# Optimization experiments

Hardware: AMD Instinct MI355X
Metric: run time of the kernel (lower is better)

Reference implementation:

```python
import jax, jax.numpy as jnp
import numpy as np

B, S, D, H = 2, 2048, 1024, 16
DK = D // H  # 64


def setup_inputs() -> dict:
    key = jax.random.key(0)
    ks = jax.random.split(key, 8)
    q = jax.random.normal(ks[0], (B, S, D), dtype=jnp.float32)
    k = jax.random.normal(ks[1], (B, S, D), dtype=jnp.float32)
    v = jax.random.normal(ks[2], (B, S, D), dtype=jnp.float32)
    mask = jax.random.randint(ks[3], (B, 1, S, S), 0, 2, dtype=jnp.int32)
    scale = 1.0 / np.sqrt(D)
    Wq = jax.random.normal(ks[4], (D, D), dtype=jnp.float32) * scale
    Wk = jax.random.normal(ks[5], (D, D), dtype=jnp.float32) * scale
    Wv = jax.random.normal(ks[6], (D, D), dtype=jnp.float32) * scale
    Wo = jax.random.normal(ks[7], (D, D), dtype=jnp.float32) * scale
    return {"q": q, "k": k, "v": v, "mask": mask,
            "Wq": Wq, "Wk": Wk, "Wv": Wv, "Wo": Wo}


def reference(q, k, v, mask, Wq, Wk, Wv, Wo):
    # Linear projections (torch nn.Linear: x @ W.T, no bias)
    qh = (q @ Wq.T).reshape(B, S, H, DK).transpose(0, 2, 1, 3)  # [B,H,S,DK]
    kh = (k @ Wk.T).reshape(B, S, H, DK).transpose(0, 2, 1, 3)
    vh = (v @ Wv.T).reshape(B, S, H, DK).transpose(0, 2, 1, 3)
    # Scaled dot-product attention with mask fill of -1e9 where mask == 0
    scores = jnp.einsum('bhqd,bhkd->bhqk', qh, kh) / jnp.sqrt(jnp.float32(DK))
    scores = jnp.where(mask == 0, jnp.float32(-1e9), scores)
    attn = jax.nn.softmax(scores, axis=-1)
    ctx = jnp.einsum('bhqk,bhkd->bhqd', attn, vh)  # [B,H,S,DK]
    ctx = ctx.transpose(0, 2, 1, 3).reshape(B, S, D)
    return ctx @ Wo.T
```

## Files before the change

### kernel.cpp

```cpp
#include <hip/hip_runtime.h>

using u16    = unsigned short;
using u32    = unsigned int;
using f32x4  = __attribute__((ext_vector_type(4))) float;
using f32x16 = __attribute__((ext_vector_type(16))) float;
using bf16x8 = __attribute__((ext_vector_type(8))) __bf16;
using u16x4  = __attribute__((ext_vector_type(4))) u16;
using u16x8  = __attribute__((ext_vector_type(8))) u16;
using u32x2  = __attribute__((ext_vector_type(2))) u32;
using u32x4  = __attribute__((ext_vector_type(4))) u32;
using i32x4  = __attribute__((ext_vector_type(4))) int;


__device__ __forceinline__ u16 f2bf(float f) {
  union { __bf16 b; u16 u; } c; c.b = (__bf16)f; return c.u;
}

typedef __attribute__((address_space(1))) const void GVoid;
typedef __attribute__((address_space(3))) void LVoid;

__device__ __forceinline__ void gload_lds16(const void* g, void* l) {
  __builtin_amdgcn_global_load_lds((GVoid*)g, (LVoid*)l, 16, 0, 0);
}

__global__ void cvt_w(const float* __restrict__ a, const float* __restrict__ b,
                      const float* __restrict__ c, const float* __restrict__ dd,
                      u16* __restrict__ oa, u16* __restrict__ ob,
                      u16* __restrict__ oc, u16* __restrict__ od) {
  int y = blockIdx.y;
  const float* s = (y == 0) ? a : (y == 1) ? b : (y == 2) ? c : dd;
  u16* d = (y == 0) ? oa : (y == 1) ? ob : (y == 2) ? oc : od;
  int i = blockIdx.x * 256 + threadIdx.x;
  f32x4 v = ((const f32x4*)s)[i];
  u16x4 r;
#pragma unroll
  for (int j = 0; j < 4; ++j) r[j] = f2bf(v[j]);
  ((u16x4*)d)[i] = r;
}

__global__ void pack_mask(const int* __restrict__ m, u32* __restrict__ mp) {
  int tid = blockIdx.x * 256 + threadIdx.x;
  int q = tid & 2047, kt = (tid >> 11) & 31, b = tid >> 16;
  const i32x4* src = (const i32x4*)(m + ((size_t)(b * 2048 + q)) * 2048 + kt * 64);
  u32 w0 = 0, w1 = 0;
#pragma unroll
  for (int j = 0; j < 8; ++j) {
    i32x4 a = src[j], c = src[j + 8];
#pragma unroll
    for (int e = 0; e < 4; ++e) {
      w0 |= (a[e] != 0 ? 1u : 0u) << (j * 4 + e);
      w1 |= (c[e] != 0 ? 1u : 0u) << (j * 4 + e);
    }
  }
  ((u32x2*)mp)[((size_t)(b * 32 + kt)) * 2048 + q] = u32x2{w0, w1};
}

__global__ __launch_bounds__(256, 3) void gemm_qkv(const float* __restrict__ Aq,
                                                   const float* __restrict__ Ak,
                                                   const float* __restrict__ Av,
                                                   const u16* __restrict__ Wb,
                                                   u16* __restrict__ out) {
  __shared__ alignas(16) char lds[49152];
  const int t = threadIdx.x;
  const int lane = t & 63, wid = t >> 6;
  const int g = lane >> 4, r16 = lane & 15;
  const int wm = wid >> 1, wn = wid & 1;
  const int m0 = blockIdx.x * 128, n0 = blockIdx.y * 128;
  const int z = blockIdx.z;

  const float* Axf = (z == 0) ? Aq : (z == 1) ? Ak : Av;
  const char* Ab = (const char*)Axf;
  const char* Bb = (const char*)(Wb + (size_t)z * 1048576);
  u16* op = out + (size_t)z * 4194304;
  const float qsc = (z == 0) ? 0.18033688011f : 1.0f;

  f32x4 acc[4][4] = {};

  for (int kk = 0; kk < 1024; kk += 64) {
#pragma unroll
    for (int i = 0; i < 8; ++i) {
      int ci = i * 256 + t;
      int row = ci >> 4;
      int pc = ci & 15;
      int lc = pc ^ (row & 15);
      gload_lds16(Ab + (size_t)(m0 + row) * 4096 + kk * 4 + lc * 16, lds + ci * 16);
    }
#pragma unroll
    for (int i = 0; i < 4; ++i) {
      int ci = i * 256 + t;
      int row = ci >> 3;
      int cbs = ((ci & 7) << 4) ^ ((row & 7) << 4);
      gload_lds16(Bb + (size_t)(n0 + row) * 2048 + kk * 2 + cbs, lds + 32768 + ci * 16);
    }
    __syncthreads();
#pragma unroll
    for (int kc = 0; kc < 2; ++kc) {
      bf16x8 af[4], bfr[4];
#pragma unroll
      for (int mf = 0; mf < 4; ++mf) {
        int row = wm * 64 + mf * 16 + r16;
        const char* arow = lds + row * 256;
        int x = row & 15;
        int lc0 = 8 * kc + 2 * g;
        f32x4 alo = *(const f32x4*)(arow + ((lc0 ^ x) * 16));
        f32x4 ahi = *(const f32x4*)(arow + (((lc0 + 1) ^ x) * 16));
        u16x8 pk;
#pragma unroll
        for (int j = 0; j < 4; ++j) { pk[j] = f2bf(alo[j]); pk[4 + j] = f2bf(ahi[j]); }
        af[mf] = __builtin_bit_cast(bf16x8, pk);
      }
#pragma unroll
      for (int nf = 0; nf < 4; ++nf) {
        int row = wn * 64 + nf * 16 + r16;
        bfr[nf] = *(const bf16x8*)(lds + 32768 + row * 128 +
                                   ((64 * kc + 16 * g) ^ ((row & 7) << 4)));
      }
#pragma unroll
      for (int mf = 0; mf < 4; ++mf)
#pragma unroll
        for (int nf = 0; nf < 4; ++nf)
          acc[mf][nf] = __builtin_amdgcn_mfma_f32_16x16x32_bf16(af[mf], bfr[nf], acc[mf][nf], 0, 0, 0);
    }
    __syncthreads();
  }

#pragma unroll
  for (int mf = 0; mf < 4; ++mf) {
#pragma unroll
    for (int nf = 0; nf < 4; ++nf) {
      int mb = m0 + wm * 64 + mf * 16 + 4 * g;
      int n = n0 + wn * 64 + nf * 16 + r16;
      if (z == 0) {
        int bb = mb >> 11, h = n >> 6, dk = n & 63;
#pragma unroll
        for (int r = 0; r < 4; ++r) {
          int s2 = (mb + r) & 2047;
          op[((size_t)(bb * 16 + h) * 2048 + s2) * 64 + dk] = f2bf(acc[mf][nf][r] * qsc);
        }
      } else if (z == 1) {
        int h = n >> 6, dk = n & 63;
#pragma unroll
        for (int r = 0; r < 4; ++r) {
          int m = mb + r;
          int bb = m >> 11, s2 = m & 2047;
          size_t off16 = ((((size_t)(bb * 16 + h) * 32 + (s2 >> 6)) * 2 + ((s2 >> 5) & 1)) * 8 +
                          (dk >> 3)) * 32 + (s2 & 31);
          op[off16 * 8 + (dk & 7)] = f2bf(acc[mf][nf][r]);
        }
      } else {
        int bb = mb >> 11, s2 = mb & 2047, h = n >> 6, d = n & 63;
        size_t off16 = ((((size_t)(bb * 16 + h) * 32 + (s2 >> 6)) * 8 + ((s2 & 63) >> 3)) * 2 +
                        (d >> 5)) * 32 + (d & 31);
        u16x4 pv;
#pragma unroll
        for (int r = 0; r < 4; ++r) pv[r] = f2bf(acc[mf][nf][r]);
        *(u16x4*)(op + off16 * 8 + (s2 & 7)) = pv;
      }
    }
  }
}

__global__ __launch_bounds__(256, 2) void gemm_out(const u16* __restrict__ X,
                                                   const u16* __restrict__ W,
                                                   float* __restrict__ out) {
  __shared__ alignas(16) char lds[24576];
  const int t = threadIdx.x;
  const int lane = t & 63, wid = t >> 6;
  const int g = lane >> 4, r16 = lane & 15;
  const int m0 = blockIdx.x * 64, n0 = blockIdx.y * 128;
  const char* Ab = (const char*)X;
  const char* Bb = (const char*)W;

  f32x4 acc[4][2] = {};

  for (int kk = 0; kk < 1024; kk += 64) {
#pragma unroll
    for (int i = 0; i < 2; ++i) {
      int ci = i * 256 + t;
      int row = ci >> 3;
      int cbs = ((ci & 7) << 4) ^ ((row & 7) << 4);
      gload_lds16(Ab + (size_t)(m0 + row) * 2048 + kk * 2 + cbs, lds + ci * 16);
    }
#pragma unroll
    for (int i = 0; i < 4; ++i) {
      int ci = i * 256 + t;
      int row = ci >> 3;
      int cbs = ((ci & 7) << 4) ^ ((row & 7) << 4);
      gload_lds16(Bb + (size_t)(n0 + row) * 2048 + kk * 2 + cbs, lds + 8192 + ci * 16);
    }
    __syncthreads();
#pragma unroll
    for (int kc = 0; kc < 2; ++kc) {
      bf16x8 af[4], bfr[2];
#pragma unroll
      for (int mf = 0; mf < 4; ++mf) {
        int row = mf * 16 + r16;
        af[mf] = *(const bf16x8*)(lds + row * 128 + ((64 * kc + 16 * g) ^ ((row & 7) << 4)));
      }
#pragma unroll
      for (int nf = 0; nf < 2; ++nf) {
        int row = wid * 32 + nf * 16 + r16;
        bfr[nf] = *(const bf16x8*)(lds + 8192 + row * 128 + ((64 * kc + 16 * g) ^ ((row & 7) << 4)));
      }
#pragma unroll
      for (int mf = 0; mf < 4; ++mf)
#pragma unroll
        for (int nf = 0; nf < 2; ++nf)
          acc[mf][nf] = __builtin_amdgcn_mfma_f32_16x16x32_bf16(af[mf], bfr[nf], acc[mf][nf], 0, 0, 0);
    }
    __syncthreads();
  }

#pragma unroll
  for (int mf = 0; mf < 4; ++mf)
#pragma unroll
    for (int nf = 0; nf < 2; ++nf) {
      int mb = m0 + mf * 16 + 4 * g;
      int n = n0 + wid * 32 + nf * 16 + r16;
#pragma unroll
      for (int r = 0; r < 4; ++r) out[(size_t)(mb + r) * 1024 + n] = acc[mf][nf][r];
    }
}

struct KH { bf16x8 k[4]; };

__device__ __forceinline__ void loadKh(KH& f, const char* p) {
#pragma unroll
  for (int c = 0; c < 4; ++c) f.k[c] = *(const bf16x8*)(p + c * 1024);
}

__device__ __forceinline__ void sm_cvt(f32x16& s, u32 wm, float& lr, u32 (&w)[8]) {
  float ps = 0.f;
#pragma unroll
  for (int r = 0; r < 16; ++r) {
    const int bit = (r & 3) + 8 * (r >> 2);
    float p = __builtin_amdgcn_exp2f(s[r]);
    int sm = ((int)(wm << (31 - bit))) >> 31;
    p = __uint_as_float(__float_as_uint(p) & (u32)sm);
    s[r] = p;
    ps += p;
  }
  lr += ps;
#pragma unroll
  for (int ss = 0; ss < 2; ++ss) {
    u32 A0, B0, A1, B1;
    asm("v_cvt_pk_bf16_f32 %0, %1, %2" : "=v"(A0) : "v"(s[8*ss+0]), "v"(s[8*ss+1]));
    asm("v_cvt_pk_bf16_f32 %0, %1, %2" : "=v"(B0) : "v"(s[8*ss+2]), "v"(s[8*ss+3]));
    asm("v_cvt_pk_bf16_f32 %0, %1, %2" : "=v"(A1) : "v"(s[8*ss+4]), "v"(s[8*ss+5]));
    asm("v_cvt_pk_bf16_f32 %0, %1, %2" : "=v"(B1) : "v"(s[8*ss+6]), "v"(s[8*ss+7]));
    asm("v_permlane32_swap_b32 %0, %1" : "+v"(A0), "+v"(A1));
    asm("v_permlane32_swap_b32 %0, %1" : "+v"(B0), "+v"(B1));
    w[4*ss+0] = A0; w[4*ss+1] = B0; w[4*ss+2] = A1; w[4*ss+3] = B1;
  }
}

__device__ __forceinline__ void attn_body(const bf16x8 (&qfa)[4], const bf16x8 (&qfb)[4],
                                          KH& cur, KH& nxt,
                                          const char*& kp, const char*& vp,
                                          const u32x2*& mpa, const u32x2*& mpb,
                                          u32x2& mca, u32x2& mcb,
                                          int kh, int hi,
                                          f32x16& oa0, f32x16& oa1,
                                          f32x16& ob0, f32x16& ob1,
                                          float& lra, float& lrb) {
  bf16x8 v00 = *(const bf16x8*)(vp);
  bf16x8 v01 = *(const bf16x8*)(vp + 512);
  bf16x8 v10 = *(const bf16x8*)(vp + 2048);
  bf16x8 v11 = *(const bf16x8*)(vp + 2560);
  loadKh(nxt, kp);
  u32x2 mna = *mpa;
  u32x2 mnb = *mpb;
  kp += 8192; vp += 8192; mpa += 2048; mpb += 2048;
  __builtin_amdgcn_sched_barrier(0);

  f32x16 sa = {}, sb = {};
#pragma unroll
  for (int c = 0; c < 4; ++c) {
    sa = __builtin_amdgcn_mfma_f32_32x32x16_bf16(cur.k[c], qfa[c], sa, 0, 0, 0);
    sb = __builtin_amdgcn_mfma_f32_32x32x16_bf16(cur.k[c], qfb[c], sb, 0, 0, 0);
  }

  u32 wma = (kh ? mca.y : mca.x) >> (4 * hi);
  u32 wmb = (kh ? mcb.y : mcb.x) >> (4 * hi);
  u32 wa[8], wb[8];
  sm_cvt(sa, wma, lra, wa);
  sm_cvt(sb, wmb, lrb, wb);

  bf16x8 pa0 = __builtin_bit_cast(bf16x8, u32x4{wa[0], wa[1], wa[2], wa[3]});
  bf16x8 pa1 = __builtin_bit_cast(bf16x8, u32x4{wa[4], wa[5], wa[6], wa[7]});
  bf16x8 pb0 = __builtin_bit_cast(bf16x8, u32x4{wb[0], wb[1], wb[2], wb[3]});
  bf16x8 pb1 = __builtin_bit_cast(bf16x8, u32x4{wb[4], wb[5], wb[6], wb[7]});
  oa0 = __builtin_amdgcn_mfma_f32_32x32x16_bf16(pa0, v00, oa0, 0, 0, 0);
  ob0 = __builtin_amdgcn_mfma_f32_32x32x16_bf16(pb0, v00, ob0, 0, 0, 0);
  oa1 = __builtin_amdgcn_mfma_f32_32x32x16_bf16(pa0, v01, oa1, 0, 0, 0);
  ob1 = __builtin_amdgcn_mfma_f32_32x32x16_bf16(pb0, v01, ob1, 0, 0, 0);
  oa0 = __builtin_amdgcn_mfma_f32_32x32x16_bf16(pa1, v10, oa0, 0, 0, 0);
  ob0 = __builtin_amdgcn_mfma_f32_32x32x16_bf16(pb1, v10, ob0, 0, 0, 0);
  oa1 = __builtin_amdgcn_mfma_f32_32x32x16_bf16(pa1, v11, oa1, 0, 0, 0);
  ob1 = __builtin_amdgcn_mfma_f32_32x32x16_bf16(pb1, v11, ob1, 0, 0, 0);
  mca = mna;
  mcb = mnb;
}

__global__ __launch_bounds__(256, 2) void attn_kern(const u16* __restrict__ Qh,
                                                    const u16* __restrict__ Kh,
                                                    const u16* __restrict__ Vt,
                                                    const u32* __restrict__ mp,
                                                    u16* __restrict__ ctx) {
  __shared__ float cmb[2][2][32][64];
  __shared__ float cmbl[2][2][64];
  const int t = threadIdx.x;
  const int wid = t >> 6, lane = t & 63;
  const int qw = wid & 1, kh = wid >> 1;
  const int hi = lane >> 5, l31 = lane & 31;

  const int wg = (blockIdx.x & 7) * 64 + (blockIdx.x >> 3);
  const int qt = wg & 15, bh = wg >> 4;
  const int b = bh >> 4, h = bh & 15;

  const char* qbytes = (const char*)Qh;
  const int qbase_a = qt * 128 + qw * 64;
  const int qbase_b = qbase_a + 32;
  const int qga = qbase_a + l31;
  const int qgb = qbase_b + l31;

  bf16x8 qfa[4], qfb[4];
#pragma unroll
  for (int c = 0; c < 4; ++c) {
    qfa[c] = *(const bf16x8*)(qbytes + ((size_t)bh * 2048 + qga) * 128 + 32 * c + 16 * hi);
    qfb[c] = *(const bf16x8*)(qbytes + ((size_t)bh * 2048 + qgb) * 128 + 32 * c + 16 * hi);
  }

  const char* kp = (const char*)Kh + (size_t)bh * 262144 + kh * 4096 + hi * 512 + l31 * 16;
  const char* vp = (const char*)Vt + (size_t)bh * 262144 + (size_t)(4 * kh + hi) * 1024 + l31 * 16;
  const u32x2* mpa = (const u32x2*)mp + (size_t)b * 65536 + qga;
  const u32x2* mpb = (const u32x2*)mp + (size_t)b * 65536 + qgb;

  f32x16 oa0 = {}, oa1 = {}, ob0 = {}, ob1 = {};
  float lra = 0.f, lrb = 0.f;

  KH A, B2;
  loadKh(A, kp);
  kp += 8192;
  u32x2 mca = *mpa;
  u32x2 mcb = *mpb;
  mpa += 2048; mpb += 2048;

#pragma unroll 1
  for (int it = 0; it < 16; ++it) {
    attn_body(qfa, qfb, A, B2, kp, vp, mpa, mpb, mca, mcb, kh, hi, oa0, oa1, ob0, ob1, lra, lrb);
    attn_body(qfa, qfb, B2, A, kp, vp, mpa, mpb, mca, mcb, kh, hi, oa0, oa1, ob0, ob1, lra, lrb);
  }

  lra += __shfl_xor(lra, 32, 64);
  lrb += __shfl_xor(lrb, 32, 64);

  if (kh) {
#pragma unroll
    for (int r = 0; r < 16; ++r) {
      cmb[qw][0][r][lane]      = oa0[r];
      cmb[qw][0][16 + r][lane] = oa1[r];
      cmb[qw][1][r][lane]      = ob0[r];
      cmb[qw][1][16 + r][lane] = ob1[r];
    }
    cmbl[qw][0][lane] = lra;
    cmbl[qw][1][lane] = lrb;
  }
  __syncthreads();
  if (!kh) {
#pragma unroll
    for (int r = 0; r < 16; ++r) {
      oa0[r] += cmb[qw][0][r][lane];
      oa1[r] += cmb[qw][0][16 + r][lane];
      ob0[r] += cmb[qw][1][r][lane];
      ob1[r] += cmb[qw][1][16 + r][lane];
    }
    lra += cmbl[qw][0][lane];
    lrb += cmbl[qw][1][lane];

    float rla = 1.f / lra, rlb = 1.f / lrb;
#pragma unroll
    for (int r = 0; r < 16; ++r) {
      int crow = (r & 3) + 8 * (r >> 2) + 4 * hi;
      float rva = __shfl(rla, crow, 64);
      float rvb = __shfl(rlb, crow, 64);
      size_t rowa = ((size_t)b * 2048 + qbase_a + crow) * 1024 + h * 64 + l31;
      size_t rowb = ((size_t)b * 2048 + qbase_b + crow) * 1024 + h * 64 + l31;
      ctx[rowa]      = f2bf(oa0[r] * rva);
      ctx[rowa + 32] = f2bf(oa1[r] * rva);
      ctx[rowb]      = f2bf(ob0[r] * rvb);
      ctx[rowb + 32] = f2bf(ob1[r] * rvb);
    }
  }
}

extern "C" void kernel_launch(void* const* d_in, const int* in_sizes, int n_in,
                              void* d_out, int out_size, void* d_ws, size_t ws_size,
                              hipStream_t stream) {
  const float* q  = (const float*)d_in[0];
  const float* k  = (const float*)d_in[1];
  const float* v  = (const float*)d_in[2];
  const int* mask = (const int*)d_in[3];
  const float* Wq = (const float*)d_in[4];
  const float* Wk = (const float*)d_in[5];
  const float* Wv = (const float*)d_in[6];
  const float* Wo = (const float*)d_in[7];

  u16* ws = (u16*)d_ws;
  const size_t NX = (size_t)4096 * 1024;
  const size_t NW = (size_t)1024 * 1024;
  u16* Wqb = ws + 3 * NX;
  u16* Qh  = Wqb + 4 * NW;
  u16* ctx = Qh + 3 * NX;
  u32* mpk = (u32*)ws;

  cvt_w<<<dim3(1024, 4), 256, 0, stream>>>(Wq, Wk, Wv, Wo,
                                           Wqb, Wqb + NW, Wqb + 2 * NW, Wqb + 3 * NW);
  pack_mask<<<dim3(512), 256, 0, stream>>>(mask, mpk);
  gemm_qkv<<<dim3(32, 8, 3), 256, 0, stream>>>(q, k, v, Wqb, Qh);
  attn_kern<<<dim3(512), 256, 0, stream>>>(Qh, Qh + NX, Qh + 2 * NX, mpk, ctx);
  gemm_out<<<dim3(64, 8), 256, 0, stream>>>(ctx, Wqb + 3 * NW, (float*)d_out);
}
```

Measured before the change: 119.3 us.

## Pre-convert Q/K/V activations to bf16 before the QKV projection GEMM

Activations q, k and v are converted to bf16 in a merged conversion kernel together with the weights, and the QKV GEMM now loads bf16 tiles for both operands. This halves the A-tile LDS footprint and global traffic inside the GEMM and removes the per-fragment fp32-to-bf16 packing in its inner loop. In exchange the conversion pass writes and re-reads an extra 24MB of bf16 activations. The workspace region shared with the packed mask is reused, so pack_mask is moved after the GEMM. Launch bounds drop from 3 to 2 blocks per SM.

```diff
diff --git a/kernel.cpp b/kernel.cpp
--- a/kernel.cpp
+++ b/kernel.cpp
@@ -23,19 +23,31 @@
   __builtin_amdgcn_global_load_lds((GVoid*)g, (LVoid*)l, 16, 0, 0);
 }
 
-__global__ void cvt_w(const float* __restrict__ a, const float* __restrict__ b,
-                      const float* __restrict__ c, const float* __restrict__ dd,
-                      u16* __restrict__ oa, u16* __restrict__ ob,
-                      u16* __restrict__ oc, u16* __restrict__ od) {
-  int y = blockIdx.y;
-  const float* s = (y == 0) ? a : (y == 1) ? b : (y == 2) ? c : dd;
-  u16* d = (y == 0) ? oa : (y == 1) ? ob : (y == 2) ? oc : od;
-  int i = blockIdx.x * 256 + threadIdx.x;
-  f32x4 v = ((const f32x4*)s)[i];
+__global__ void cvt_all(const float* __restrict__ q, const float* __restrict__ k,
+                        const float* __restrict__ v, const float* __restrict__ wq,
+                        const float* __restrict__ wk, const float* __restrict__ wv,
+                        const float* __restrict__ wo,
+                        u16* __restrict__ oq, u16* __restrict__ ok, u16* __restrict__ ov,
+                        u16* __restrict__ owq, u16* __restrict__ owk,
+                        u16* __restrict__ owv, u16* __restrict__ owo) {
+  size_t u = (size_t)blockIdx.x * 256 + threadIdx.x;
+  const float* s; u16* d; size_t off;
+  int sel = (int)(u >> 20);
+  if (sel < 3) {
+    s = sel == 0 ? q : sel == 1 ? k : v;
+    d = sel == 0 ? oq : sel == 1 ? ok : ov;
+    off = u & 1048575;
+  } else {
+    int wsel = (int)(u >> 18) & 3;
+    s = wsel == 0 ? wq : wsel == 1 ? wk : wsel == 2 ? wv : wo;
+    d = wsel == 0 ? owq : wsel == 1 ? owk : wsel == 2 ? owv : owo;
+    off = u & 262143;
+  }
+  f32x4 x = ((const f32x4*)s)[off];
   u16x4 r;
 #pragma unroll
-  for (int j = 0; j < 4; ++j) r[j] = f2bf(v[j]);
-  ((u16x4*)d)[i] = r;
+  for (int j = 0; j < 4; ++j) r[j] = f2bf(x[j]);
+  ((u16x4*)d)[off] = r;
 }
 
 __global__ void pack_mask(const int* __restrict__ m, u32* __restrict__ mp) {
@@ -55,12 +67,10 @@
   ((u32x2*)mp)[((size_t)(b * 32 + kt)) * 2048 + q] = u32x2{w0, w1};
 }
 
-__global__ __launch_bounds__(256, 3) void gemm_qkv(const float* __restrict__ Aq,
-                                                   const float* __restrict__ Ak,
-                                                   const float* __restrict__ Av,
-                                                   const u16* __restrict__ Wb,
+__global__ __launch_bounds__(256, 2) void gemm_qkv(const u16* __restrict__ X,
+                                                   const u16* __restrict__ W,
                                                    u16* __restrict__ out) {
-  __shared__ alignas(16) char lds[49152];
+  __shared__ alignas(16) char lds[32768];
   const int t = threadIdx.x;
   const int lane = t & 63, wid = t >> 6;
   const int g = lane >> 4, r16 = lane & 15;
@@ -68,29 +78,21 @@
   const int m0 = blockIdx.x * 128, n0 = blockIdx.y * 128;
   const int z = blockIdx.z;
 
-  const float* Axf = (z == 0) ? Aq : (z == 1) ? Ak : Av;
-  const char* Ab = (const char*)Axf;
-  const char* Bb = (const char*)(Wb + (size_t)z * 1048576);
+  const char* Ab = (const char*)(X + (size_t)z * 4194304);
+  const char* Bb = (const char*)(W + (size_t)z * 1048576);
   u16* op = out + (size_t)z * 4194304;
   const float qsc = (z == 0) ? 0.18033688011f : 1.0f;
 
   f32x4 acc[4][4] = {};
 
   for (int kk = 0; kk < 1024; kk += 64) {
-#pragma unroll
-    for (int i = 0; i < 8; ++i) {
-      int ci = i * 256 + t;
-      int row = ci >> 4;
-      int pc = ci & 15;
-      int lc = pc ^ (row & 15);
-      gload_lds16(Ab + (size_t)(m0 + row) * 4096 + kk * 4 + lc * 16, lds + ci * 16);
-    }
 #pragma unroll
     for (int i = 0; i < 4; ++i) {
       int ci = i * 256 + t;
       int row = ci >> 3;
       int cbs = ((ci & 7) << 4) ^ ((row & 7) << 4);
-      gload_lds16(Bb + (size_t)(n0 + row) * 2048 + kk * 2 + cbs, lds + 32768 + ci * 16);
+      gload_lds16(Ab + (size_t)(m0 + row) * 2048 + kk * 2 + cbs, lds + ci * 16);
+      gload_lds16(Bb + (size_t)(n0 + row) * 2048 + kk * 2 + cbs, lds + 16384 + ci * 16);
     }
     __syncthreads();
 #pragma unroll
@@ -99,21 +101,12 @@
 #pragma unroll
       for (int mf = 0; mf < 4; ++mf) {
         int row = wm * 64 + mf * 16 + r16;
-        const char* arow = lds + row * 256;
-        int x = row & 15;
-        int lc0 = 8 * kc + 2 * g;
-        f32x4 alo = *(const f32x4*)(arow + ((lc0 ^ x) * 16));
-        f32x4 ahi = *(const f32x4*)(arow + (((lc0 + 1) ^ x) * 16));
-        u16x8 pk;
-#pragma unroll
-        for (int j = 0; j < 4; ++j) { pk[j] = f2bf(alo[j]); pk[4 + j] = f2bf(ahi[j]); }
-        af[mf] = __builtin_bit_cast(bf16x8, pk);
+        af[mf] = *(const bf16x8*)(lds + row * 128 + ((64 * kc + 16 * g) ^ ((row & 7) << 4)));
       }
 #pragma unroll
       for (int nf = 0; nf < 4; ++nf) {
         int row = wn * 64 + nf * 16 + r16;
-        bfr[nf] = *(const bf16x8*)(lds + 32768 + row * 128 +
-                                   ((64 * kc + 16 * g) ^ ((row & 7) << 4)));
+        bfr[nf] = *(const bf16x8*)(lds + 16384 + row * 128 + ((64 * kc + 16 * g) ^ ((row & 7) << 4)));
       }
 #pragma unroll
       for (int mf = 0; mf < 4; ++mf)
@@ -409,15 +402,17 @@
   u16* ws = (u16*)d_ws;
   const size_t NX = (size_t)4096 * 1024;
   const size_t NW = (size_t)1024 * 1024;
+  u16* Xq  = ws;
   u16* Wqb = ws + 3 * NX;
   u16* Qh  = Wqb + 4 * NW;
   u16* ctx = Qh + 3 * NX;
   u32* mpk = (u32*)ws;
 
-  cvt_w<<<dim3(1024, 4), 256, 0, stream>>>(Wq, Wk, Wv, Wo,
+  cvt_all<<<dim3(16384), 256, 0, stream>>>(q, k, v, Wq, Wk, Wv, Wo,
+                                           Xq, Xq + NX, Xq + 2 * NX,
                                            Wqb, Wqb + NW, Wqb + 2 * NW, Wqb + 3 * NW);
+  gemm_qkv<<<dim3(32, 8, 3), 256, 0, stream>>>(Xq, Wqb, Qh);
   pack_mask<<<dim3(512), 256, 0, stream>>>(mask, mpk);
-  gemm_qkv<<<dim3(32, 8, 3), 256, 0, stream>>>(q, k, v, Wqb, Qh);
   attn_kern<<<dim3(512), 256, 0, stream>>>(Qh, Qh + NX, Qh + 2 * NX, mpk, ctx);
   gemm_out<<<dim3(64, 8), 256, 0, stream>>>(ctx, Wqb + 3 * NW, (float*)d_out);
 }
```

New measurement: 120.6 us. No clear change (+1.1%).
